# Performance work log

Measured on AMD Instinct MI355X. Metric: run time of the kernel, lower is better.

The kernel has to match this reference:

```python
import jax, jax.numpy as jnp
import numpy as np

TAU = 1.0
K = 10
N_NODES = 1048576
N_GRAPHS = 4096


def setup_inputs() -> dict:
    key = jax.random.key(0)
    k1, k2, k3 = jax.random.split(key, 3)
    # per-node scalar logits
    x = jax.random.normal(k1, (N_NODES, 1), dtype=jnp.float32)
    # uniforms for gumbel noise, kept away from {0,1} for log stability
    uniforms = jax.random.uniform(k2, (N_NODES, 3 * K), dtype=jnp.float32,
                                  minval=1e-6, maxval=1.0 - 1e-6)
    # PyG-style ptr: B+1 cumulative offsets, ptr[0]=0, ptr[-1]=N
    cuts = jnp.sort(jax.random.randint(k3, (N_GRAPHS - 1,), 1, N_NODES))
    ptr = jnp.concatenate([jnp.zeros((1,), cuts.dtype), cuts,
                           jnp.full((1,), N_NODES, cuts.dtype)])
    return {"x": x, "uniforms": uniforms, "ptr": ptr}


def reference(x, uniforms, ptr):
    # x: [N, 1] node logits; uniforms: [N, 3k]; ptr: [B+1] segment offsets
    N = x.shape[0]
    B = ptr.shape[0] - 1
    # node i belongs to graph g where ptr[g] <= i < ptr[g+1]
    seg = jnp.searchsorted(ptr, jnp.arange(N), side="right") - 1  # [N]
    gumbel = -jnp.log(-jnp.log(uniforms))                           # [N, 3k]
    noisy = (gumbel + x) / TAU                                      # [N, 3k]
    # segmented softmax over nodes (dim=0 within each graph), per column
    m = jax.ops.segment_max(noisy, seg, num_segments=B)             # [B, 3k]
    e = jnp.exp(noisy - m[seg])                                     # [N, 3k]
    denom = jax.ops.segment_sum(e, seg, num_segments=B)             # [B, 3k]
    probs = e / denom[seg]                                          # [N, 3k]
    # max over the 3k gumbel samples per node
    samples = jnp.max(probs, axis=1)                                # [N]
    return samples[:, None]                                         # [N, 1]
```

## Files before the change

### kernel.cpp

```cpp
#include <hip/hip_runtime.h>

#define NK3 30
#define NKP 15

__device__ __forceinline__ float hw_log2(float a) { return __builtin_amdgcn_logf(a); }
__device__ __forceinline__ float hw_exp2(float a) { return __builtin_amdgcn_exp2f(a); }
__device__ __forceinline__ float hw_rcp(float a)  { return __builtin_amdgcn_rcpf(a); }


__global__ __launch_bounds__(256) void k0_zero(float4* __restrict__ ws, int count4)
{
    const int i = blockIdx.x * 256 + threadIdx.x;
    if (i < count4) ws[i] = make_float4(0.f, 0.f, 0.f, 0.f);
}

__global__ __launch_bounds__(256) void k1_accumulate(
    const float* __restrict__ x, const float* __restrict__ uniforms,
    const int* __restrict__ ptr, float* __restrict__ wsum, int N, int B)
{
    const int wid  = (blockIdx.x << 2) + (threadIdx.x >> 6);
    const int lane = threadIdx.x & 63;
    const int nodesub = lane >> 4;
    const int cp      = lane & 15;
    const bool active = cp < NKP;
    const int cpl     = active ? cp : 0;

    const int base = wid << 7;
    if (base >= N) return;

    const int n0 = base + nodesub;
    int lo = 0, hi = B;
    while (hi - lo > 1) { int mid = (lo + hi) >> 1; if (ptr[mid] <= n0) lo = mid; else hi = mid; }
    int seg = lo;
    int ptr_next = ptr[seg + 1];

    float ax = 0.f, ay = 0.f;

    for (int s8 = 0; s8 < 4; ++s8) {
        float2 u[8];
        float  xv[8];
#pragma unroll
        for (int q = 0; q < 8; ++q) {
            const int n = base + (s8 << 5) + (q << 2) + nodesub;
            const int nc = (n < N) ? n : (N - 1);
            u[q]  = reinterpret_cast<const float2*>(uniforms + (size_t)nc * NK3)[cpl];
            xv[q] = x[nc];
        }
#pragma unroll
        for (int q = 0; q < 8; ++q) {
            const int n = base + (s8 << 5) + (q << 2) + nodesub;
            if (n < N) {
                if (n >= ptr_next) {
                    if (active) {
                        atomicAdd(&wsum[seg * NK3 + (cp << 1)    ], ax);
                        atomicAdd(&wsum[seg * NK3 + (cp << 1) + 1], ay);
                    }
                    ax = 0.f; ay = 0.f;
                    do { ++seg; ptr_next = ptr[seg + 1]; } while (n >= ptr_next);
                }
                const float E  = hw_exp2(xv[q] * 1.44269504f);
                const float w0 = -hw_log2(u[q].x);
                const float w1 = -hw_log2(u[q].y);
                ax = fmaf(E, hw_rcp(w0), ax);
                ay = fmaf(E, hw_rcp(w1), ay);
            }
        }
    }
    if (active) {
        atomicAdd(&wsum[seg * NK3 + (cp << 1)    ], ax);
        atomicAdd(&wsum[seg * NK3 + (cp << 1) + 1], ay);
    }
}

__global__ __launch_bounds__(256) void k3_output(
    const float* __restrict__ x, const float* __restrict__ uniforms,
    const int* __restrict__ ptr, const float* __restrict__ den,
    float* __restrict__ out, int N, int B)
{
    const int wid  = (blockIdx.x << 2) + (threadIdx.x >> 6);
    const int lane = threadIdx.x & 63;
    const int base = wid << 8;
    if (base >= N) return;

    const int n0 = base + lane;
    int lo = 0, hi = B;
    while (hi - lo > 1) { int mid = (lo + hi) >> 1; if (ptr[mid] <= n0) lo = mid; else hi = mid; }
    int seg = lo;

    for (int c = 0; c < 4; ++c) {
        const int n = base + (c << 6) + lane;
        if (n >= N) return;
        while (n >= ptr[seg + 1]) ++seg;

        float l[NK3];
#pragma unroll
        for (int j = 0; j < NK3; ++j) l[j] = hw_rcp(den[seg * NK3 + j]);

        const float2* row = reinterpret_cast<const float2*>(uniforms + (size_t)n * NK3);
        float mx = 0.0f;
#pragma unroll
        for (int k = 0; k < NKP; ++k) {
            const float2 u = row[k];
            const float r0 = hw_rcp(-hw_log2(u.x));
            const float r1 = hw_rcp(-hw_log2(u.y));
            mx = fmaxf(mx, fmaxf(r0 * l[2 * k], r1 * l[2 * k + 1]));
        }
        out[n] = hw_exp2(x[n] * 1.44269504f) * mx;
    }
}

__global__ __launch_bounds__(256) void gnn_fallback(
    const float* __restrict__ x, const float* __restrict__ uniforms,
    const int* __restrict__ ptr, float* __restrict__ out)
{
    const int wave = threadIdx.x >> 6;
    const int lane = threadIdx.x & 63;
    const int g = (blockIdx.x << 2) + wave;
    const int start = ptr[g];
    const int end   = ptr[g + 1];
    if (end <= start) return;

    float acc[NK3];
#pragma unroll
    for (int j = 0; j < NK3; ++j) acc[j] = 0.0f;
    const int iters = (end - start + 63) >> 6;

    for (int it = 0; it < iters; ++it) {
        const int n = start + (it << 6) + lane;
        if (n < end) {
            const float E = hw_exp2(x[n] * 1.44269504f);
            const float2* row = reinterpret_cast<const float2*>(uniforms + (size_t)n * NK3);
#pragma unroll
            for (int k = 0; k < NKP; ++k) {
                float2 u = row[k];
                acc[2 * k]     = fmaf(E, hw_rcp(-hw_log2(u.x)), acc[2 * k]);
                acc[2 * k + 1] = fmaf(E, hw_rcp(-hw_log2(u.y)), acc[2 * k + 1]);
            }
        }
    }
#pragma unroll
    for (int j = 0; j < NK3; ++j) {
        float v = acc[j];
#pragma unroll
        for (int off = 1; off < 64; off <<= 1) v += __shfl_xor(v, off, 64);
        acc[j] = hw_rcp(v);
    }
    for (int it = 0; it < iters; ++it) {
        const int n = start + (it << 6) + lane;
        if (n < end) {
            const float2* row = reinterpret_cast<const float2*>(uniforms + (size_t)n * NK3);
            float mx = 0.0f;
#pragma unroll
            for (int k = 0; k < NKP; ++k) {
                float2 u = row[k];
                const float r0 = hw_rcp(-hw_log2(u.x));
                const float r1 = hw_rcp(-hw_log2(u.y));
                mx = fmaxf(mx, fmaxf(r0 * acc[2 * k], r1 * acc[2 * k + 1]));
            }
            out[n] = hw_exp2(x[n] * 1.44269504f) * mx;
        }
    }
}

extern "C" void kernel_launch(void* const* d_in, const int* in_sizes, int n_in,
                              void* d_out, int out_size, void* d_ws, size_t ws_size,
                              hipStream_t stream) {
    const float* x        = (const float*)d_in[0];
    const float* uniforms = (const float*)d_in[1];
    const int*   ptr      = (const int*)d_in[2];
    float* out = (float*)d_out;

    const int N = in_sizes[0];
    const int B = in_sizes[2] - 1;
    const size_t ws_needed = (size_t)B * NK3 * sizeof(float);

    if (ws_size >= ws_needed && d_ws != nullptr) {
        float* wsum = (float*)d_ws;

        const int cnt  = B * NK3;
        const int cnt4 = cnt >> 2;
        const int b0 = (cnt4 + 255) / 256;
        k0_zero<<<b0, 256, 0, stream>>>((float4*)wsum, cnt4);

        const int b1 = (N + 511) / 512;
        k1_accumulate<<<b1, 256, 0, stream>>>(x, uniforms, ptr, wsum, N, B);

        const int b3 = (N + 1023) / 1024;
        k3_output<<<b3, 256, 0, stream>>>(x, uniforms, ptr, wsum, out, N, B);
    } else {
        const int blocks = (B + 3) / 4;
        gnn_fallback<<<blocks, 256, 0, stream>>>(x, uniforms, ptr, out);
    }
}
```

Measured before the change: 83.39 us.

## Assign one node per lane in accumulate kernel with wave-wide shuffle reductions

The accumulate kernel now maps one node per lane, with each lane loading its full 30-column uniform row. Per-segment sums are formed by butterfly shuffle reductions across the wave for each segment the wave spans, followed by one atomic per column. This replaces the earlier layout of 16 lanes per node with a serial per-lane scan over 32 nodes. The per-lane row loads are strided and less coalesced, and each wave now runs 30×6 shuffles per segment it touches, which can add up when segments are short.

```diff
diff --git a/kernel.cpp b/kernel.cpp
--- a/kernel.cpp
+++ b/kernel.cpp
@@ -20,55 +20,47 @@
 {
     const int wid  = (blockIdx.x << 2) + (threadIdx.x >> 6);
     const int lane = threadIdx.x & 63;
-    const int nodesub = lane >> 4;
-    const int cp      = lane & 15;
-    const bool active = cp < NKP;
-    const int cpl     = active ? cp : 0;
-
-    const int base = wid << 7;
+    const int base = wid << 6;
     if (base >= N) return;
 
-    const int n0 = base + nodesub;
+    const int n  = base + lane;
+    const int nv = (n < N) ? n : (N - 1);
+    const bool valid = (n < N);
+
     int lo = 0, hi = B;
-    while (hi - lo > 1) { int mid = (lo + hi) >> 1; if (ptr[mid] <= n0) lo = mid; else hi = mid; }
-    int seg = lo;
-    int ptr_next = ptr[seg + 1];
+    while (hi - lo > 1) { int mid = (lo + hi) >> 1; if (ptr[mid] <= nv) lo = mid; else hi = mid; }
+    const int seg = lo;
 
-    float ax = 0.f, ay = 0.f;
+    const float2* row = reinterpret_cast<const float2*>(uniforms + (size_t)nv * NK3);
+    float2 u[NKP];
+#pragma unroll
+    for (int k = 0; k < NKP; ++k) u[k] = row[k];
+    const float E = hw_exp2(x[nv] * 1.44269504f);
 
-    for (int s8 = 0; s8 < 4; ++s8) {
-        float2 u[8];
-        float  xv[8];
+    float r[NK3];
 #pragma unroll
-        for (int q = 0; q < 8; ++q) {
-            const int n = base + (s8 << 5) + (q << 2) + nodesub;
-            const int nc = (n < N) ? n : (N - 1);
-            u[q]  = reinterpret_cast<const float2*>(uniforms + (size_t)nc * NK3)[cpl];
-            xv[q] = x[nc];
+    for (int k = 0; k < NKP; ++k) {
+        r[2 * k]     = E * hw_rcp(-hw_log2(u[k].x));
+        r[2 * k + 1] = E * hw_rcp(-hw_log2(u[k].y));
+    }
+
+    const int s_lo = __shfl(seg, 0, 64);
+    const int s_hi = __shfl(seg, 63, 64);
+
+    for (int s = s_lo; s <= s_hi; ++s) {
+        const bool mine = valid && (seg == s);
+        float v[NK3];
+#pragma unroll
+        for (int j = 0; j < NK3; ++j) v[j] = mine ? r[j] : 0.0f;
+#pragma unroll
+        for (int j = 0; j < NK3; ++j) {
+#pragma unroll
+            for (int off = 1; off < 64; off <<= 1)
+                v[j] += __shfl_xor(v[j], off, 64);
         }
 #pragma unroll
-        for (int q = 0; q < 8; ++q) {
-            const int n = base + (s8 << 5) + (q << 2) + nodesub;
-            if (n < N) {
-                if (n >= ptr_next) {
-                    if (active) {
-                        atomicAdd(&wsum[seg * NK3 + (cp << 1)    ], ax);
-                        atomicAdd(&wsum[seg * NK3 + (cp << 1) + 1], ay);
-                    }
-                    ax = 0.f; ay = 0.f;
-                    do { ++seg; ptr_next = ptr[seg + 1]; } while (n >= ptr_next);
-                }
-                const float E  = hw_exp2(xv[q] * 1.44269504f);
-                const float w0 = -hw_log2(u[q].x);
-                const float w1 = -hw_log2(u[q].y);
-                ax = fmaf(E, hw_rcp(w0), ax);
-                ay = fmaf(E, hw_rcp(w1), ay);
-            }
-        }
-    }
-    if (active) {
-        atomicAdd(&wsum[seg * NK3 + (cp << 1)    ], ax);
-        atomicAdd(&wsum[seg * NK3 + (cp << 1) + 1], ay);
+        for (int j = 0; j < NK3; ++j)
+            if (lane == j) atomicAdd(&wsum[(size_t)s * NK3 + j], v[j]);
     }
 }
 
@@ -182,7 +174,8 @@
         const int b0 = (cnt4 + 255) / 256;
         k0_zero<<<b0, 256, 0, stream>>>((float4*)wsum, cnt4);
 
-        const int b1 = (N + 511) / 512;
+        const int waves1 = (N + 63) / 64;
+        const int b1 = (waves1 + 3) / 4;
         k1_accumulate<<<b1, 256, 0, stream>>>(x, uniforms, ptr, wsum, N, B);
 
         const int b3 = (N + 1023) / 1024;
```

Measured after the change: 113.4 us. +36.0%, slower.
